# Kernel optimization log

Measured on AMD Instinct MI355X. Metric: run time of the kernel, lower is better.

The kernel has to match this reference:

```python
import jax, jax.numpy as jnp
import numpy as np

RATIOS = [0.9, 0.7, 0.5, 0.3]
EPS = 1e-5


def _layernorm(x, g, b):
    m = jnp.mean(x, axis=-1, keepdims=True)
    v = jnp.mean(jnp.square(x - m), axis=-1, keepdims=True)
    return (x - m) * jax.lax.rsqrt(v + EPS) * g + b


def _stage(x, g, b, W, bias):
    return _layernorm(x, g, b) @ W + bias


def _prune(x, W1, b1, W2, b2, ratio):
    B, N, C = x.shape
    stats = jnp.mean(x, axis=1)                       # (B, C)
    scores = jax.nn.relu(stats @ W1 + b1) @ W2 + b2    # (B, C)
    k = max(1, int(C * ratio))
    _, idx = jax.lax.top_k(jax.lax.stop_gradient(scores), k)  # (B, k)
    hard = jnp.zeros((B, C), scores.dtype).at[jnp.arange(B)[:, None], idx].set(1.0)
    soft = jax.nn.sigmoid(scores)
    # straight-through: forward value == hard, gradient flows through soft
    mask = hard + soft - jax.lax.stop_gradient(soft)
    return x * mask[:, None, :]


def setup_inputs() -> dict:
    key = jax.random.key(0)
    dims = [(96, 96), (96, 192), (192, 384), (384, 768)]
    inp = {}
    ks = jax.random.split(key, 64)
    ki = iter(ks)
    inp["x"] = jax.random.normal(next(ki), (32, 3136, 96), dtype=jnp.float32)
    for i, (din, dout) in enumerate(dims, 1):
        inp[f"s{i}_g"] = jnp.ones((din,), jnp.float32)
        inp[f"s{i}_b"] = jnp.zeros((din,), jnp.float32)
        inp[f"s{i}_W"] = jax.random.normal(next(ki), (din, dout), jnp.float32) * 0.02
        inp[f"s{i}_bias"] = jnp.zeros((dout,), jnp.float32)
        d = dout
        inp[f"p{i}_W1"] = jax.random.normal(next(ki), (d, d // 4), jnp.float32) * 0.02
        inp[f"p{i}_b1"] = jnp.zeros((d // 4,), jnp.float32)
        inp[f"p{i}_W2"] = jax.random.normal(next(ki), (d // 4, d), jnp.float32) * 0.02
        inp[f"p{i}_b2"] = jnp.zeros((d,), jnp.float32)
    inp["H"] = 56
    inp["W"] = 56
    return inp


def reference(x,
              s1_g, s1_b, s1_W, s1_bias, p1_W1, p1_b1, p1_W2, p1_b2,
              s2_g, s2_b, s2_W, s2_bias, p2_W1, p2_b1, p2_W2, p2_b2,
              s3_g, s3_b, s3_W, s3_bias, p3_W1, p3_b1, p3_W2, p3_b2,
              s4_g, s4_b, s4_W, s4_bias, p4_W1, p4_b1, p4_W2, p4_b2,
              H, W):
    x = _stage(x, s1_g, s1_b, s1_W, s1_bias)
    x = _prune(x, p1_W1, p1_b1, p1_W2, p1_b2, RATIOS[0])
    x = _stage(x, s2_g, s2_b, s2_W, s2_bias)
    x = _prune(x, p2_W1, p2_b1, p2_W2, p2_b2, RATIOS[1])
    x = _stage(x, s3_g, s3_b, s3_W, s3_bias)
    x = _prune(x, p3_W1, p3_b1, p3_W2, p3_b2, RATIOS[2])
    x = _stage(x, s4_g, s4_b, s4_W, s4_bias)
    x = _prune(x, p4_W1, p4_b1, p4_W2, p4_b2, RATIOS[3])
    return x
```

## Files before the change

### kernel.cpp

```cpp
#include <hip/hip_runtime.h>
#include <hip/hip_bf16.h>
#include <stdint.h>

#define NTOK 3136
#define MTOT 100352
#define RPW  14
#define WPB  224

typedef __attribute__((ext_vector_type(8))) short bf16x8;
typedef __attribute__((ext_vector_type(4))) float f32x4;
typedef __attribute__((ext_vector_type(2))) float f32x2;

static __device__ __forceinline__ ushort f2bf(float x) {
  union { float f; uint32_t u; } c; c.f = x;
  uint32_t r = (c.u + 0x7FFFu + ((c.u >> 16) & 1u)) >> 16;
  return (ushort)r;
}
static __device__ __forceinline__ float bf2f(ushort h) {
  union { uint32_t u; float f; } c; c.u = ((uint32_t)h) << 16;
  return c.f;
}

template<int DIN, bool WLO>
__global__ __launch_bounds__(256)
void ln_colsum_k(const float* __restrict__ in, const float* __restrict__ gma,
                 const float* __restrict__ bta, ushort* __restrict__ oh,
                 ushort* __restrict__ ol, float* __restrict__ part)
{
  constexpr int P2 = DIN / 2;
  constexpr int T2 = (P2 + 63) / 64;
  const int wid  = (blockIdx.x * 256 + threadIdx.x) >> 6;
  const int lane = threadIdx.x & 63;
  const int b = wid / WPB;
  const int w = wid - b * WPB;

  f32x2 gv[T2], bv[T2], acc[T2];
#pragma unroll
  for (int t = 0; t < T2; ++t) {
    int c2 = lane + 64 * t;
    if (c2 < P2) {
      gv[t] = *(const f32x2*)(gma + 2 * c2);
      bv[t] = *(const f32x2*)(bta + 2 * c2);
    } else { gv[t] = {0.f, 0.f}; bv[t] = {0.f, 0.f}; }
    acc[t] = {0.f, 0.f};
  }

  const size_t rbase = ((size_t)b * NTOK + (size_t)w * RPW) * DIN;
  const float* ip = in + rbase;
  ushort* oph = oh + rbase;
  ushort* opl = ol + rbase;

  for (int j = 0; j < RPW; ++j) {
    f32x2 v[T2];
    float s = 0.f, sq = 0.f;
#pragma unroll
    for (int t = 0; t < T2; ++t) {
      int c2 = lane + 64 * t;
      f32x2 xv = {0.f, 0.f};
      if (c2 < P2) xv = *(const f32x2*)(ip + (size_t)j * DIN + 2 * c2);
      v[t] = xv;
      s  += xv[0] + xv[1];
      sq += xv[0] * xv[0] + xv[1] * xv[1];
    }
#pragma unroll
    for (int off = 1; off < 64; off <<= 1) {
      s  += __shfl_xor(s, off);
      sq += __shfl_xor(sq, off);
    }
    float m   = s / (float)DIN;
    float var = sq / (float)DIN - m * m;
    float r   = 1.f / sqrtf(var + 1e-5f);
#pragma unroll
    for (int t = 0; t < T2; ++t) {
      int c2 = lane + 64 * t;
      if (c2 < P2) {
        float xn0 = (v[t][0] - m) * r * gv[t][0] + bv[t][0];
        float xn1 = (v[t][1] - m) * r * gv[t][1] + bv[t][1];
        ushort h0 = f2bf(xn0), h1 = f2bf(xn1);
        ((uint32_t*)(oph + (size_t)j * DIN))[c2] =
            (uint32_t)h0 | ((uint32_t)h1 << 16);
        if (WLO) {
          ushort l0 = f2bf(xn0 - bf2f(h0)), l1 = f2bf(xn1 - bf2f(h1));
          ((uint32_t*)(opl + (size_t)j * DIN))[c2] =
              (uint32_t)l0 | ((uint32_t)l1 << 16);
        }
        acc[t][0] += xn0;
        acc[t][1] += xn1;
      }
    }
  }
#pragma unroll
  for (int t = 0; t < T2; ++t) {
    int c2 = lane + 64 * t;
    if (c2 < P2) {
      int c = 2 * c2;
      part[((size_t)b * DIN + c) * WPB + w]     = acc[t][0];
      part[((size_t)b * DIN + c + 1) * WPB + w] = acc[t][1];
    }
  }
}

template<int DIN, int DOUT, int SLOTS>
__global__ __launch_bounds__(1024)
void scores_k(const float* __restrict__ part,
              const float* __restrict__ Wt, const float* __restrict__ bias,
              const float* __restrict__ W1, const float* __restrict__ b1,
              const float* __restrict__ W2, const float* __restrict__ b2,
              float* __restrict__ mask, int k)
{
  constexpr int DH  = DOUT / 4;
  constexpr int DH4 = DH / 4;
  constexpr int NSLC = (1024 / DH4 < 64) ? 1024 / DH4 : 64;
  constexpr int RPSC = (DOUT + NSLC - 1) / NSLC;
  constexpr int C4  = DOUT / 4;
  constexpr int NSLD = (1024 / C4 < 64) ? 1024 / C4 : 64;
  constexpr int RPSD = (DH + NSLD - 1) / NSLD;

  __shared__ float xm[DIN];
  __shared__ float st[DOUT];
  __shared__ float h[DH];
  __shared__ float sc[DOUT];
  __shared__ float red[4096];

  const int b = blockIdx.x, tid = threadIdx.x;

  if constexpr (SLOTS == 25) {
    if (tid < DIN) {
      const float* p = part + ((size_t)b * DIN + tid) * 25;
      float s = 0.f;
#pragma unroll
      for (int i = 0; i < 25; ++i) s += p[i];
      xm[tid] = s * (1.f / (float)NTOK);
    }
  } else {
    const int cg = tid >> 2, wq = tid & 3;
    if (cg < DIN) {
      const float* p = part + ((size_t)b * DIN + cg) * WPB + wq * 56;
      f32x4 a = {0.f, 0.f, 0.f, 0.f};
#pragma unroll
      for (int u = 0; u < 14; ++u) {
        f32x4 t0 = *(const f32x4*)(p + u * 4);
        a[0] += t0[0]; a[1] += t0[1]; a[2] += t0[2]; a[3] += t0[3];
      }
      red[wq * DIN + cg] = (a[0] + a[1]) + (a[2] + a[3]);
    }
    __syncthreads();
    if (tid < DIN)
      xm[tid] = ((red[0 * DIN + tid] + red[1 * DIN + tid]) +
                 (red[2 * DIN + tid] + red[3 * DIN + tid])) * (1.f / (float)NTOK);
  }
  __syncthreads();

  {
    constexpr int RPS = DIN / 4;
    const int j4 = tid % C4, sl = tid / C4;
    if (sl < 4) {
      const float* wp = Wt + (size_t)(sl * RPS) * DOUT + j4 * 4;
      f32x4 acc = {0.f, 0.f, 0.f, 0.f};
#pragma unroll
      for (int r = 0; r < RPS; ++r) {
        f32x4 wv = *(const f32x4*)(wp + (size_t)r * DOUT);
        float xv = xm[sl * RPS + r];
        acc[0] = fmaf(xv, wv[0], acc[0]);
        acc[1] = fmaf(xv, wv[1], acc[1]);
        acc[2] = fmaf(xv, wv[2], acc[2]);
        acc[3] = fmaf(xv, wv[3], acc[3]);
      }
      *(f32x4*)&red[sl * DOUT + j4 * 4] = acc;
    }
  }
  __syncthreads();
  if (tid < DOUT)
    st[tid] = ((red[0 * DOUT + tid] + red[1 * DOUT + tid]) +
               (red[2 * DOUT + tid] + red[3 * DOUT + tid])) + bias[tid];
  __syncthreads();

  {
    const int j4 = tid % DH4, sl = tid / DH4;
    if (sl < NSLC) {
      f32x4 acc = {0.f, 0.f, 0.f, 0.f};
#pragma unroll
      for (int rr = 0; rr < RPSC; ++rr) {
        int r = sl * RPSC + rr;
        if (r < DOUT) {
          f32x4 wv = *(const f32x4*)(W1 + (size_t)r * DH + j4 * 4);
          float sv = st[r];
          acc[0] = fmaf(sv, wv[0], acc[0]);
          acc[1] = fmaf(sv, wv[1], acc[1]);
          acc[2] = fmaf(sv, wv[2], acc[2]);
          acc[3] = fmaf(sv, wv[3], acc[3]);
        }
      }
      *(f32x4*)&red[(size_t)sl * DH + j4 * 4] = acc;
    }
  }
  __syncthreads();
  if (tid < DH) {
    float a = 0.f;
#pragma unroll 4
    for (int sl = 0; sl < NSLC; ++sl) a += red[(size_t)sl * DH + tid];
    h[tid] = fmaxf(b1[tid] + a, 0.f);
  }
  __syncthreads();

  {
    const int c4 = tid % C4, sl = tid / C4;
    if (sl < NSLD) {
      f32x4 acc = {0.f, 0.f, 0.f, 0.f};
#pragma unroll
      for (int rr = 0; rr < RPSD; ++rr) {
        int r = sl * RPSD + rr;
        if (r < DH) {
          f32x4 wv = *(const f32x4*)(W2 + (size_t)r * DOUT + c4 * 4);
          float hv = h[r];
          acc[0] = fmaf(hv, wv[0], acc[0]);
          acc[1] = fmaf(hv, wv[1], acc[1]);
          acc[2] = fmaf(hv, wv[2], acc[2]);
          acc[3] = fmaf(hv, wv[3], acc[3]);
        }
      }
      *(f32x4*)&red[(size_t)sl * DOUT + c4 * 4] = acc;
    }
  }
  __syncthreads();
  for (int c = tid; c < DOUT; c += 1024) {
    float a = 0.f;
#pragma unroll 4
    for (int sl = 0; sl < NSLD; ++sl) a += red[(size_t)sl * DOUT + c];
    sc[c] = b2[c] + a;
  }
  __syncthreads();

  for (int c = tid; c < DOUT; c += 1024) {
    float v = sc[c];
    int rank = 0;
#pragma unroll 8
    for (int j = 0; j < DOUT; ++j) {
      float u = sc[j];
      rank += (u > v) || (u == v && j < c);
    }
    mask[(size_t)b * DOUT + c] = (rank < k) ? 1.f : 0.f;
  }
}

__global__ __launch_bounds__(256)
void convW_all_k(const float* __restrict__ W0, const float* __restrict__ W1,
                 const float* __restrict__ W2, const float* __restrict__ W3,
                 ushort* __restrict__ hi, ushort* __restrict__ lo)
{
  const int Kd[4]   = { 96, 96, 192, 384 };
  const int Nd[4]   = { 96, 192, 384, 768 };
  const int off[5]  = { 0, 12288, 36864, 110592, 405504 };
  const float* Wp[4] = { W0, W1, W2, W3 };

  int idx = blockIdx.x * 256 + threadIdx.x;
  if (idx >= 405504) return;
  int s = (idx >= off[1]) + (idx >= off[2]) + (idx >= off[3]);
  int local = idx - off[s];
  int K = Kd[s], N = Nd[s];
  int n = local / K, kk = local - n * K;
  float v = (n < N) ? Wp[s][(size_t)kk * N + n] : 0.f;
  ushort h = f2bf(v);
  hi[idx] = h;
  lo[idx] = f2bf(v - bf2f(h));
}

#define ASYNC16(GP, LP) __builtin_amdgcn_global_load_lds( \
    (const __attribute__((address_space(1))) void*)(GP),  \
    (__attribute__((address_space(3))) void*)(LP), 16, 0, 0)

template<int K, int NSEG, int BNL, int N, int NWN, bool WLO>
__global__ __launch_bounds__(128 * NWN)
void gemm_ln_k(const ushort* __restrict__ a0, const ushort* __restrict__ a1,
               const ushort* __restrict__ a2,
               const ushort* __restrict__ b0, const ushort* __restrict__ b1,
               const ushort* __restrict__ b2,
               const float* __restrict__ bias, const float* __restrict__ msk,
               const float* __restrict__ gnext, const float* __restrict__ bnext,
               ushort* __restrict__ oh, ushort* __restrict__ ol,
               float* __restrict__ part)
{
  constexpr int T   = 128 * NWN;
  constexpr int R   = T / 4;
  constexpr int AI  = 128 / R;
  constexpr int BI  = BNL / R;
  constexpr int IS  = AI + BI;
  constexpr int WN  = N / NWN;
  constexpr int NFR = WN / 16;
  constexpr int KSTEPS = K / 32;
  constexpr int NT  = NSEG * KSTEPS;
  __shared__ __align__(16) ushort ldsA[3][128 * 32];
  __shared__ __align__(16) ushort ldsB[3][BNL * 32];

  const int tid  = threadIdx.x;
  const int lane = tid & 63;
  const int wid  = tid >> 6;
  const int wm = wid & 1, wn = wid >> 1;

  const int q8  = gridDim.x >> 3;
  const int bid = blockIdx.x;
  const int mt  = (bid & 7) * q8 + (bid >> 3);
  const size_t row0 = (size_t)mt * 128;

  const ushort* Aseg[3] = { a0, a1, a2 };
  const ushort* Bseg[3] = { b0, b1, b2 };

  f32x4 acc[4][NFR];
#pragma unroll
  for (int i = 0; i < 4; ++i)
#pragma unroll
    for (int j = 0; j < NFR; ++j) acc[i][j] = { 0.f, 0.f, 0.f, 0.f };

  const int c_row  = tid >> 2;
  const int c_phys = tid & 3;

#define STAGEF(BUF, TT)                                                        \
  {                                                                            \
    const int seg_ = (TT) / KSTEPS;                                            \
    const int k0_  = ((TT) % KSTEPS) * 32;                                     \
    const ushort* ap_ = Aseg[seg_];                                            \
    const ushort* bp_ = Bseg[seg_];                                            \
    _Pragma("unroll")                                                          \
    for (int r_ = 0; r_ < AI; ++r_) {                                          \
      int row_  = c_row + r_ * R;                                              \
      int slot_ = c_phys ^ ((row_ >> 1) & 3);                                  \
      ASYNC16(ap_ + (row0 + row_) * (size_t)K + (k0_ + slot_ * 8),             \
              &ldsA[BUF][(row_ * 4 + c_phys) * 8]);                            \
    }                                                                          \
    _Pragma("unroll")                                                          \
    for (int r_ = 0; r_ < BI; ++r_) {                                          \
      int row_  = c_row + r_ * R;                                              \
      int slot_ = c_phys ^ ((row_ >> 1) & 3);                                  \
      ASYNC16(bp_ + (size_t)row_ * K + (k0_ + slot_ * 8),                      \
              &ldsB[BUF][(row_ * 4 + c_phys) * 8]);                            \
    }                                                                          \
  }

  STAGEF(0, 0);
  STAGEF(1, 1);
#pragma unroll
  for (int t = 0; t < NT; ++t) {
    if (t == NT - 1)            { asm volatile("s_waitcnt vmcnt(0)" ::: "memory"); }
    else if constexpr (IS == 4) { asm volatile("s_waitcnt vmcnt(4)" ::: "memory"); }
    else                        { asm volatile("s_waitcnt vmcnt(5)" ::: "memory"); }
    __builtin_amdgcn_s_barrier();
    if (t + 2 < NT) STAGEF((t + 2) % 3, t + 2);
    const int buf = t % 3;
    const int slot = lane >> 4;
    const int r16  = lane & 15;
    bf16x8 af[4], bfr[NFR];
#pragma unroll
    for (int mi = 0; mi < 4; ++mi) {
      int r = wm * 64 + mi * 16 + r16;
      af[mi] = *(const bf16x8*)&ldsA[buf][(r * 4 + (slot ^ ((r >> 1) & 3))) * 8];
    }
#pragma unroll
    for (int ni = 0; ni < NFR; ++ni) {
      int r = wn * WN + ni * 16 + r16;
      bfr[ni] = *(const bf16x8*)&ldsB[buf][(r * 4 + (slot ^ ((r >> 1) & 3))) * 8];
    }
#pragma unroll
    for (int mi = 0; mi < 4; ++mi)
#pragma unroll
      for (int ni = 0; ni < NFR; ++ni)
        acc[mi][ni] = __builtin_amdgcn_mfma_f32_16x16x32_bf16(af[mi], bfr[ni],
                                                              acc[mi][ni], 0, 0, 0);
  }
#undef STAGEF

  __syncthreads();

  float* rowred = (float*)&ldsA[0][0];
  float* colred = rowred + NWN * 256;
  ushort* xsh = (ushort*)&ldsB[0][0];
  ushort* xsl = xsh + 32 * N;

  const int l15 = lane & 15, l4 = lane >> 4;
  const int b0i = (int)(row0 / NTOK);
  const size_t rowB = (size_t)(b0i + 1) * NTOK;
  const bool strad = rowB < row0 + 128;

  float biasv[NFR], mk0a[NFR], mk1a[NFR], gvn[NFR], bvn[NFR];
#pragma unroll
  for (int ni = 0; ni < NFR; ++ni) {
    int n = wn * WN + ni * 16 + l15;
    biasv[ni] = bias[n];
    mk0a[ni] = msk[(size_t)b0i * N + n];
    mk1a[ni] = strad ? msk[(size_t)(b0i + 1) * N + n] : mk0a[ni];
    gvn[ni] = gnext[n];
    bvn[ni] = bnext[n];
  }

  float rs[16], rq[16];
#pragma unroll
  for (int i = 0; i < 16; ++i) { rs[i] = 0.f; rq[i] = 0.f; }
#pragma unroll
  for (int mi = 0; mi < 4; ++mi)
#pragma unroll
    for (int q = 0; q < 4; ++q) {
      size_t row = row0 + wm * 64 + mi * 16 + l4 * 4 + q;
      bool loB = row < rowB;
#pragma unroll
      for (int ni = 0; ni < NFR; ++ni) {
        float v = (acc[mi][ni][q] + biasv[ni]) * (loB ? mk0a[ni] : mk1a[ni]);
        acc[mi][ni][q] = v;
        rs[mi * 4 + q] += v;
        rq[mi * 4 + q] += v * v;
      }
    }
#pragma unroll
  for (int off = 1; off < 16; off <<= 1)
#pragma unroll
    for (int i = 0; i < 16; ++i) {
      rs[i] += __shfl_xor(rs[i], off);
      rq[i] += __shfl_xor(rq[i], off);
    }
  if (l15 == 0) {
#pragma unroll
    for (int mi = 0; mi < 4; ++mi)
#pragma unroll
      for (int q = 0; q < 4; ++q) {
        int r = wm * 64 + mi * 16 + l4 * 4 + q;
        rowred[(wn * 128 + r) * 2 + 0] = rs[mi * 4 + q];
        rowred[(wn * 128 + r) * 2 + 1] = rq[mi * 4 + q];
      }
  }
  __syncthreads();

  float mean[16], rstd[16];
#pragma unroll
  for (int mi = 0; mi < 4; ++mi)
#pragma unroll
    for (int q = 0; q < 4; ++q) {
      int r = wm * 64 + mi * 16 + l4 * 4 + q;
      float S = 0.f, Q = 0.f;
#pragma unroll
      for (int w = 0; w < NWN; ++w) {
        S += rowred[(w * 128 + r) * 2 + 0];
        Q += rowred[(w * 128 + r) * 2 + 1];
      }
      float mn  = S / (float)N;
      float var = Q / (float)N - mn * mn;
      mean[mi * 4 + q] = mn;
      rstd[mi * 4 + q] = 1.f / sqrtf(var + 1e-5f);
    }

  float cs0[NFR], cs1[NFR];
#pragma unroll
  for (int ni = 0; ni < NFR; ++ni) { cs0[ni] = 0.f; cs1[ni] = 0.f; }
#pragma unroll
  for (int mi = 0; mi < 4; ++mi) {
    __syncthreads();
#pragma unroll
    for (int q = 0; q < 4; ++q) {
      const int rl = l4 * 4 + q;
      const size_t row = row0 + wm * 64 + mi * 16 + rl;
      const bool loB = row < rowB;
      const float mn = mean[mi * 4 + q], rv = rstd[mi * 4 + q];
#pragma unroll
      for (int ni = 0; ni < NFR; ++ni) {
        const int n = wn * WN + ni * 16 + l15;
        float xn = (acc[mi][ni][q] - mn) * rv * gvn[ni] + bvn[ni];
        ushort hh = f2bf(xn);
        xsh[(wm * 16 + rl) * N + n] = hh;
        if constexpr (WLO) xsl[(wm * 16 + rl) * N + n] = f2bf(xn - bf2f(hh));
        if (loB) cs0[ni] += xn; else cs1[ni] += xn;
      }
    }
    __syncthreads();
    constexpr int U4R = N / 8;
    for (int idx = tid; idx < 32 * U4R; idx += T) {
      const int grp = idx / U4R, c = idx - grp * U4R;
      const size_t row = row0 + (grp >> 4) * 64 + mi * 16 + (grp & 15);
      *(uint4*)(oh + row * (size_t)N + c * 8) =
          *(const uint4*)(xsh + grp * N + c * 8);
      if constexpr (WLO)
        *(uint4*)(ol + row * (size_t)N + c * 8) =
            *(const uint4*)(xsl + grp * N + c * 8);
    }
  }

#pragma unroll
  for (int ni = 0; ni < NFR; ++ni) {
    cs0[ni] += __shfl_xor(cs0[ni], 16);
    cs0[ni] += __shfl_xor(cs0[ni], 32);
    cs1[ni] += __shfl_xor(cs1[ni], 16);
    cs1[ni] += __shfl_xor(cs1[ni], 32);
  }
  __syncthreads();
  if (l4 == 0) {
#pragma unroll
    for (int ni = 0; ni < NFR; ++ni) {
      int n = wn * WN + ni * 16 + l15;
      colred[(0 * 2 + wm) * N + n] = cs0[ni];
      colred[(1 * 2 + wm) * N + n] = cs1[ni];
    }
  }
  __syncthreads();
  if (wm == 0 && l4 == 0) {
    const int mt_lo = (b0i * NTOK) >> 7;
    const int slot0 = mt - mt_lo;
#pragma unroll
    for (int ni = 0; ni < NFR; ++ni) {
      int n = wn * WN + ni * 16 + l15;
      float t0 = colred[0 * N + n] + colred[1 * N + n];
      part[((size_t)b0i * N + n) * 25 + slot0] = t0;
      if (strad) {
        float t1 = colred[2 * N + n] + colred[3 * N + n];
        part[((size_t)(b0i + 1) * N + n) * 25 + 0] = t1;
      }
    }
  }
}

template<int K, int NSEG, int BN>
__global__ __launch_bounds__(256)
void gemm_mfma_k(const ushort* __restrict__ a0, const ushort* __restrict__ a1,
                 const ushort* __restrict__ a2,
                 const ushort* __restrict__ b0, const ushort* __restrict__ b1,
                 const ushort* __restrict__ b2,
                 const float* __restrict__ bias, const float* __restrict__ msk,
                 float* __restrict__ C, int N)
{
  constexpr int KSTEPS = K / 32;
  constexpr int NT  = NSEG * KSTEPS;
  constexpr int WN  = BN / 2;
  constexpr int NFR = WN / 16;
  constexpr int BR  = BN / 64;
  __shared__ __align__(16) ushort ldsA[3][128 * 32];
  __shared__ __align__(16) ushort ldsB[3][BN * 32];

  const int tid  = threadIdx.x;
  const int lane = tid & 63;
  const int wid  = tid >> 6;
  const int wm = wid >> 1, wn = wid & 1;

  const int NBN = (N + BN - 1) / BN;
  const int q8  = gridDim.x >> 3;
  const int bid = blockIdx.x;
  const int wg  = (bid & 7) * q8 + (bid >> 3);
  const int mt  = wg / NBN;
  const int nt  = wg - mt * NBN;
  const size_t row0 = (size_t)mt * 128;
  const int n0 = nt * BN;

  const ushort* Aseg[3] = { a0, a1, a2 };
  const ushort* Bseg[3] = { b0, b1, b2 };

  f32x4 acc[4][NFR];
#pragma unroll
  for (int i = 0; i < 4; ++i)
#pragma unroll
    for (int j = 0; j < NFR; ++j) acc[i][j] = { 0.f, 0.f, 0.f, 0.f };

  const int c_row  = tid >> 2;
  const int c_phys = tid & 3;

#define STAGE4(BUF, TT)                                                        \
  {                                                                            \
    const int seg_ = (TT) / KSTEPS;                                            \
    const int k0_  = ((TT) % KSTEPS) * 32;                                     \
    const ushort* ap_ = Aseg[seg_];                                            \
    const ushort* bp_ = Bseg[seg_];                                            \
    _Pragma("unroll")                                                          \
    for (int r_ = 0; r_ < 2; ++r_) {                                           \
      int row_  = c_row + r_ * 64;                                             \
      int slot_ = c_phys ^ ((row_ >> 1) & 3);                                  \
      ASYNC16(ap_ + (row0 + row_) * (size_t)K + (k0_ + slot_ * 8),             \
              &ldsA[BUF][(row_ * 4 + c_phys) * 8]);                            \
    }                                                                          \
    _Pragma("unroll")                                                          \
    for (int r_ = 0; r_ < BR; ++r_) {                                          \
      int row_  = c_row + r_ * 64;                                             \
      int slot_ = c_phys ^ ((row_ >> 1) & 3);                                  \
      ASYNC16(bp_ + (size_t)(n0 + row_) * K + (k0_ + slot_ * 8),               \
              &ldsB[BUF][(row_ * 4 + c_phys) * 8]);                            \
    }                                                                          \
  }

  STAGE4(0, 0);
  STAGE4(1, 1);
#pragma unroll
  for (int t = 0; t < NT; ++t) {
    if (t == NT - 1)              { asm volatile("s_waitcnt vmcnt(0)" ::: "memory"); }
    else if constexpr (BN == 128) { asm volatile("s_waitcnt vmcnt(4)" ::: "memory"); }
    else if constexpr (BN == 192) { asm volatile("s_waitcnt vmcnt(5)" ::: "memory"); }
    else                          { asm volatile("s_waitcnt vmcnt(6)" ::: "memory"); }
    __builtin_amdgcn_s_barrier();
    if (t + 2 < NT) STAGE4((t + 2) % 3, t + 2);
    const int buf = t % 3;
    const int slot = lane >> 4;
    const int r16  = lane & 15;
    bf16x8 af[4], bfr[NFR];
#pragma unroll
    for (int mi = 0; mi < 4; ++mi) {
      int r = wm * 64 + mi * 16 + r16;
      af[mi] = *(const bf16x8*)&ldsA[buf][(r * 4 + (slot ^ ((r >> 1) & 3))) * 8];
    }
#pragma unroll
    for (int ni = 0; ni < NFR; ++ni) {
      int r = wn * WN + ni * 16 + r16;
      bfr[ni] = *(const bf16x8*)&ldsB[buf][(r * 4 + (slot ^ ((r >> 1) & 3))) * 8];
    }
#pragma unroll
    for (int mi = 0; mi < 4; ++mi)
#pragma unroll
      for (int ni = 0; ni < NFR; ++ni)
        acc[mi][ni] = __builtin_amdgcn_mfma_f32_16x16x32_bf16(af[mi], bfr[ni],
                                                              acc[mi][ni], 0, 0, 0);
  }
#undef STAGE4

  float* cst = (float*)&ldsB[0][0];

  const int l15 = lane & 15, l4 = lane >> 4;
  const int b0i = (int)(row0 / NTOK);
  const size_t rowB = (size_t)(b0i + 1) * NTOK;
  const bool straddle = (rowB < row0 + 128) && (b0i + 1 < 32);

  float biasv[NFR], mk0a[NFR], mk1a[NFR];
#pragma unroll
  for (int ni = 0; ni < NFR; ++ni) {
    int n = n0 + wn * WN + ni * 16 + l15;
    biasv[ni] = bias[n];
    mk0a[ni] = msk[(size_t)b0i * N + n];
    mk1a[ni] = straddle ? msk[(size_t)(b0i + 1) * N + n] : mk0a[ni];
  }

#pragma unroll
  for (int mi = 0; mi < 4; ++mi) {
    __syncthreads();
#pragma unroll
    for (int q = 0; q < 4; ++q) {
      const int rl = l4 * 4 + q;
      const size_t m = row0 + wm * 64 + mi * 16 + rl;
      const bool loB = m < rowB;
#pragma unroll
      for (int ni = 0; ni < NFR; ++ni) {
        const int nn = wn * WN + ni * 16 + l15;
        cst[(wm * 16 + rl) * BN + nn] =
            (acc[mi][ni][q] + biasv[ni]) * (loB ? mk0a[ni] : mk1a[ni]);
      }
    }
    __syncthreads();
    constexpr int F4R = BN / 4;
    for (int idx = tid; idx < 32 * F4R; idx += 256) {
      const int grp = idx / F4R, c = idx - grp * F4R;
      const size_t row = row0 + (grp >> 4) * 64 + mi * 16 + (grp & 15);
      *(f32x4*)(C + row * (size_t)N + n0 + c * 4) =
          *(const f32x4*)(cst + grp * BN + c * 4);
    }
  }
}

extern "C" void kernel_launch(void* const* d_in, const int* in_sizes, int n_in,
                              void* d_out, int out_size, void* d_ws, size_t ws_size,
                              hipStream_t stream)
{
  (void)in_sizes; (void)n_in; (void)out_size; (void)ws_size;
  const float* x = (const float*)d_in[0];
  const float *sg[4], *sb[4], *sW[4], *sbias[4], *pW1[4], *pb1[4], *pW2[4], *pb2[4];
  for (int s = 0; s < 4; ++s) {
    int base = 1 + s * 8;
    sg[s]    = (const float*)d_in[base + 0];
    sb[s]    = (const float*)d_in[base + 1];
    sW[s]    = (const float*)d_in[base + 2];
    sbias[s] = (const float*)d_in[base + 3];
    pW1[s]   = (const float*)d_in[base + 4];
    pb1[s]   = (const float*)d_in[base + 5];
    pW2[s]   = (const float*)d_in[base + 6];
    pb2[s]   = (const float*)d_in[base + 7];
  }

  float* out = (float*)d_out;
  ushort* hiA = (ushort*)out;
  ushort* loA = (ushort*)(out + 19267584);
  ushort* loB = (ushort*)(out + 38535168);

  char* ws = (char*)d_ws;
  ushort* hiB  = (ushort*)(ws);
  float*  part = (float*) (ws + 77070336);
  float*  mk   = (float*) (ws + 79822848);
  ushort* w_hi = (ushort*)(ws + 79921152);
  ushort* w_lo = (ushort*)(ws + 80732160);

  const int woff[4] = { 0, 12288, 36864, 110592 };

  convW_all_k<<<(405504 + 255) / 256, 256, 0, stream>>>(
      sW[0], sW[1], sW[2], sW[3], w_hi, w_lo);

  const int LNG = 32 * WPB / 4;

  ln_colsum_k<96, true><<<LNG, 256, 0, stream>>>(x, sg[0], sb[0], hiA, loA, part);
  scores_k<96, 96, 224><<<32, 1024, 0, stream>>>(part, sW[0], sbias[0],
      pW1[0], pb1[0], pW2[0], pb2[0], mk, 86);
  gemm_ln_k<96, 3, 128, 96, 2, true><<<784, 256, 0, stream>>>(
      hiA, hiA, loA, w_hi + woff[0], w_lo + woff[0], w_hi + woff[0],
      sbias[0], mk, sg[1], sb[1], hiB, loB, part);

  scores_k<96, 192, 25><<<32, 1024, 0, stream>>>(part, sW[1], sbias[1],
      pW1[1], pb1[1], pW2[1], pb2[1], mk, 134);
  gemm_ln_k<96, 3, 192, 192, 2, true><<<784, 256, 0, stream>>>(
      hiB, hiB, loB, w_hi + woff[1], w_lo + woff[1], w_hi + woff[1],
      sbias[1], mk, sg[2], sb[2], hiA, loA, part);

  scores_k<192, 384, 25><<<32, 1024, 0, stream>>>(part, sW[2], sbias[2],
      pW1[2], pb1[2], pW2[2], pb2[2], mk, 192);
  gemm_ln_k<192, 3, 384, 384, 4, false><<<784, 512, 0, stream>>>(
      hiA, hiA, loA, w_hi + woff[2], w_lo + woff[2], w_hi + woff[2],
      sbias[2], mk, sg[3], sb[3], hiB, (ushort*)nullptr, part);

  scores_k<384, 768, 25><<<32, 1024, 0, stream>>>(part, sW[3], sbias[3],
      pW1[3], pb1[3], pW2[3], pb2[3], mk, 230);
  gemm_mfma_k<384, 1, 256><<<784 * 3, 256, 0, stream>>>(
      hiB, hiB, hiB, w_hi + woff[3], w_hi + woff[3], w_hi + woff[3],
      sbias[3], mk, out, 768);
}
```

Baseline: 550.7 us.

## Compute only the selected top-k output channels in the final stage GEMM

Result: faster. 490.3 us (-11.0%).

```diff
diff --git a/kernel.cpp b/kernel.cpp
--- a/kernel.cpp
+++ b/kernel.cpp
@@ -100,13 +100,15 @@
   }
 }
 
-template<int DIN, int DOUT, int SLOTS>
+template<int DIN, int DOUT, int SLOTS, bool CMP>
 __global__ __launch_bounds__(1024)
 void scores_k(const float* __restrict__ part,
               const float* __restrict__ Wt, const float* __restrict__ bias,
               const float* __restrict__ W1, const float* __restrict__ b1,
               const float* __restrict__ W2, const float* __restrict__ b2,
-              float* __restrict__ mask, int k)
+              float* __restrict__ mask, int k,
+              const ushort* __restrict__ wsrc, ushort* __restrict__ wc,
+              int* __restrict__ list_g, float* __restrict__ biasc)
 {
   constexpr int DH  = DOUT / 4;
   constexpr int DH4 = DH / 4;
@@ -121,6 +123,7 @@
   __shared__ float h[DH];
   __shared__ float sc[DOUT];
   __shared__ float red[4096];
+  __shared__ int lsh[256];
 
   const int b = blockIdx.x, tid = threadIdx.x;
 
@@ -240,6 +243,24 @@
       rank += (u > v) || (u == v && j < c);
     }
     mask[(size_t)b * DOUT + c] = (rank < k) ? 1.f : 0.f;
+    if (CMP && rank < k) lsh[rank] = c;
+  }
+  if constexpr (CMP) {
+    if (tid >= k && tid < 256) lsh[tid] = -1;
+    __syncthreads();
+    if (tid < 256) {
+      int c = lsh[tid];
+      list_g[b * 256 + tid] = c;
+      biasc[b * 256 + tid] = (c >= 0) ? bias[c] : 0.f;
+    }
+    constexpr int U4 = 384 / 8;
+    for (int idx = tid; idx < 256 * U4; idx += 1024) {
+      int j = idx / U4, u = idx - j * U4;
+      int src = lsh[j];
+      uint4 v = make_uint4(0u, 0u, 0u, 0u);
+      if (src >= 0) v = *(const uint4*)(wsrc + (size_t)src * 384 + u * 8);
+      *(uint4*)(wc + (size_t)b * 98304 + (size_t)j * 384 + u * 8) = v;
+    }
   }
 }
 
@@ -371,9 +392,9 @@
   __syncthreads();
 
   float* rowred = (float*)&ldsA[0][0];
-  float* colred = rowred + NWN * 256;
   ushort* xsh = (ushort*)&ldsB[0][0];
   ushort* xsl = xsh + 32 * N;
+  float* colred = (float*)(xsh + 32 * N * (WLO ? 2 : 1));
 
   const int l15 = lane & 15, l4 = lane >> 4;
   const int b0i = (int)(row0 / NTOK);
@@ -513,142 +534,130 @@
   }
 }
 
-template<int K, int NSEG, int BN>
-__global__ __launch_bounds__(256)
-void gemm_mfma_k(const ushort* __restrict__ a0, const ushort* __restrict__ a1,
-                 const ushort* __restrict__ a2,
-                 const ushort* __restrict__ b0, const ushort* __restrict__ b1,
-                 const ushort* __restrict__ b2,
-                 const float* __restrict__ bias, const float* __restrict__ msk,
-                 float* __restrict__ C, int N)
+template<int K>
+__global__ __launch_bounds__(512)
+void gemm_c4_k(const ushort* __restrict__ A, const ushort* __restrict__ Wc,
+               const int* __restrict__ list, const float* __restrict__ biasc,
+               float* __restrict__ C)
 {
-  constexpr int KSTEPS = K / 32;
-  constexpr int NT  = NSEG * KSTEPS;
-  constexpr int WN  = BN / 2;
-  constexpr int NFR = WN / 16;
-  constexpr int BR  = BN / 64;
+  constexpr int NT = K / 32;
   __shared__ __align__(16) ushort ldsA[3][128 * 32];
-  __shared__ __align__(16) ushort ldsB[3][BN * 32];
+  __shared__ __align__(16) ushort ldsB[3][256 * 32];
 
   const int tid  = threadIdx.x;
   const int lane = tid & 63;
   const int wid  = tid >> 6;
-  const int wm = wid >> 1, wn = wid & 1;
-
-  const int NBN = (N + BN - 1) / BN;
+  const int wm = wid & 1, wn = wid >> 1;
+
   const int q8  = gridDim.x >> 3;
   const int bid = blockIdx.x;
   const int wg  = (bid & 7) * q8 + (bid >> 3);
-  const int mt  = wg / NBN;
-  const int nt  = wg - mt * NBN;
-  const size_t row0 = (size_t)mt * 128;
-  const int n0 = nt * BN;
-
-  const ushort* Aseg[3] = { a0, a1, a2 };
-  const ushort* Bseg[3] = { b0, b1, b2 };
-
-  f32x4 acc[4][NFR];
-#pragma unroll
-  for (int i = 0; i < 4; ++i)
-#pragma unroll
-    for (int j = 0; j < NFR; ++j) acc[i][j] = { 0.f, 0.f, 0.f, 0.f };
+  const int b   = wg / 25;
+  const int mt  = wg - b * 25;
+  const size_t row0 = (size_t)b * NTOK + (size_t)mt * 128;
+  const int rows_valid = (mt == 24) ? 64 : 128;
+
+  const ushort* bp = Wc + (size_t)b * 256 * K;
 
   const int c_row  = tid >> 2;
   const int c_phys = tid & 3;
 
-#define STAGE4(BUF, TT)                                                        \
+  size_t arow = row0 + c_row;
+  const size_t rowEnd = (size_t)(b + 1) * NTOK;
+  if (arow >= rowEnd) arow = rowEnd - 1;
+  const ushort* apr = A + arow * (size_t)K;
+
+  f32x4 acc[4][4];
+#pragma unroll
+  for (int i = 0; i < 4; ++i)
+#pragma unroll
+    for (int j = 0; j < 4; ++j) acc[i][j] = { 0.f, 0.f, 0.f, 0.f };
+
+#define STAGEC(BUF, TT)                                                        \
   {                                                                            \
-    const int seg_ = (TT) / KSTEPS;                                            \
-    const int k0_  = ((TT) % KSTEPS) * 32;                                     \
-    const ushort* ap_ = Aseg[seg_];                                            \
-    const ushort* bp_ = Bseg[seg_];                                            \
+    const int k0_ = (TT) * 32;                                                 \
+    {                                                                          \
+      int slot_ = c_phys ^ ((c_row >> 1) & 3);                                 \
+      ASYNC16(apr + (k0_ + slot_ * 8),                                         \
+              &ldsA[BUF][(c_row * 4 + c_phys) * 8]);                           \
+    }                                                                          \
     _Pragma("unroll")                                                          \
     for (int r_ = 0; r_ < 2; ++r_) {                                           \
-      int row_  = c_row + r_ * 64;                                             \
+      int row_  = c_row + r_ * 128;                                            \
       int slot_ = c_phys ^ ((row_ >> 1) & 3);                                  \
-      ASYNC16(ap_ + (row0 + row_) * (size_t)K + (k0_ + slot_ * 8),             \
-              &ldsA[BUF][(row_ * 4 + c_phys) * 8]);                            \
-    }                                                                          \
-    _Pragma("unroll")                                                          \
-    for (int r_ = 0; r_ < BR; ++r_) {                                          \
-      int row_  = c_row + r_ * 64;                                             \
-      int slot_ = c_phys ^ ((row_ >> 1) & 3);                                  \
-      ASYNC16(bp_ + (size_t)(n0 + row_) * K + (k0_ + slot_ * 8),               \
+      ASYNC16(bp + (size_t)row_ * K + (k0_ + slot_ * 8),                       \
               &ldsB[BUF][(row_ * 4 + c_phys) * 8]);                            \
     }                                                                          \
   }
 
-  STAGE4(0, 0);
-  STAGE4(1, 1);
+  STAGEC(0, 0);
+  STAGEC(1, 1);
 #pragma unroll
   for (int t = 0; t < NT; ++t) {
-    if (t == NT - 1)              { asm volatile("s_waitcnt vmcnt(0)" ::: "memory"); }
-    else if constexpr (BN == 128) { asm volatile("s_waitcnt vmcnt(4)" ::: "memory"); }
-    else if constexpr (BN == 192) { asm volatile("s_waitcnt vmcnt(5)" ::: "memory"); }
-    else                          { asm volatile("s_waitcnt vmcnt(6)" ::: "memory"); }
+    if (t == NT - 1) { asm volatile("s_waitcnt vmcnt(0)" ::: "memory"); }
+    else             { asm volatile("s_waitcnt vmcnt(3)" ::: "memory"); }
     __builtin_amdgcn_s_barrier();
-    if (t + 2 < NT) STAGE4((t + 2) % 3, t + 2);
+    if (t + 2 < NT) STAGEC((t + 2) % 3, t + 2);
     const int buf = t % 3;
     const int slot = lane >> 4;
     const int r16  = lane & 15;
-    bf16x8 af[4], bfr[NFR];
+    bf16x8 af[4], bfr[4];
 #pragma unroll
     for (int mi = 0; mi < 4; ++mi) {
       int r = wm * 64 + mi * 16 + r16;
       af[mi] = *(const bf16x8*)&ldsA[buf][(r * 4 + (slot ^ ((r >> 1) & 3))) * 8];
     }
 #pragma unroll
-    for (int ni = 0; ni < NFR; ++ni) {
-      int r = wn * WN + ni * 16 + r16;
+    for (int ni = 0; ni < 4; ++ni) {
+      int r = wn * 64 + ni * 16 + r16;
       bfr[ni] = *(const bf16x8*)&ldsB[buf][(r * 4 + (slot ^ ((r >> 1) & 3))) * 8];
     }
 #pragma unroll
     for (int mi = 0; mi < 4; ++mi)
 #pragma unroll
-      for (int ni = 0; ni < NFR; ++ni)
+      for (int ni = 0; ni < 4; ++ni)
         acc[mi][ni] = __builtin_amdgcn_mfma_f32_16x16x32_bf16(af[mi], bfr[ni],
                                                               acc[mi][ni], 0, 0, 0);
   }
-#undef STAGE4
+#undef STAGEC
 
   float* cst = (float*)&ldsB[0][0];
 
   const int l15 = lane & 15, l4 = lane >> 4;
-  const int b0i = (int)(row0 / NTOK);
-  const size_t rowB = (size_t)(b0i + 1) * NTOK;
-  const bool straddle = (rowB < row0 + 128) && (b0i + 1 < 32);
-
-  float biasv[NFR], mk0a[NFR], mk1a[NFR];
-#pragma unroll
-  for (int ni = 0; ni < NFR; ++ni) {
-    int n = n0 + wn * WN + ni * 16 + l15;
-    biasv[ni] = bias[n];
-    mk0a[ni] = msk[(size_t)b0i * N + n];
-    mk1a[ni] = straddle ? msk[(size_t)(b0i + 1) * N + n] : mk0a[ni];
-  }
-
-#pragma unroll
-  for (int mi = 0; mi < 4; ++mi) {
+  int   nj[4];
+  float biasv[4];
+#pragma unroll
+  for (int ni = 0; ni < 4; ++ni) {
+    int j = wn * 64 + ni * 16 + l15;
+    nj[ni]    = list[b * 256 + j];
+    biasv[ni] = biasc[b * 256 + j];
+  }
+
+#pragma unroll
+  for (int hh = 0; hh < 8; ++hh) {
+    const int hrows = rows_valid - hh * 16;
+    if (hrows <= 0) break;
     __syncthreads();
-#pragma unroll
-    for (int q = 0; q < 4; ++q) {
-      const int rl = l4 * 4 + q;
-      const size_t m = row0 + wm * 64 + mi * 16 + rl;
-      const bool loB = m < rowB;
-#pragma unroll
-      for (int ni = 0; ni < NFR; ++ni) {
-        const int nn = wn * WN + ni * 16 + l15;
-        cst[(wm * 16 + rl) * BN + nn] =
-            (acc[mi][ni][q] + biasv[ni]) * (loB ? mk0a[ni] : mk1a[ni]);
-      }
-    }
+    for (int idx = tid; idx < 16 * 192; idx += 512)
+      ((f32x4*)cst)[idx] = f32x4{0.f, 0.f, 0.f, 0.f};
     __syncthreads();
-    constexpr int F4R = BN / 4;
-    for (int idx = tid; idx < 32 * F4R; idx += 256) {
-      const int grp = idx / F4R, c = idx - grp * F4R;
-      const size_t row = row0 + (grp >> 4) * 64 + mi * 16 + (grp & 15);
-      *(f32x4*)(C + row * (size_t)N + n0 + c * 4) =
-          *(const f32x4*)(cst + grp * BN + c * 4);
+    if ((hh >> 2) == wm) {
+      const int mi = hh & 3;
+#pragma unroll
+      for (int q = 0; q < 4; ++q) {
+        const int rl = l4 * 4 + q;
+#pragma unroll
+        for (int ni = 0; ni < 4; ++ni)
+          if (nj[ni] >= 0)
+            cst[rl * 768 + nj[ni]] = acc[mi][ni][q] + biasv[ni];
+      }
+    }
+    __syncthreads();
+    const int nst = (hrows >= 16 ? 16 : hrows) * 192;
+    for (int idx = tid; idx < nst; idx += 512) {
+      const int grp = idx / 192, c = idx - grp * 192;
+      const size_t row = row0 + hh * 16 + grp;
+      *(f32x4*)(C + row * 768 + c * 4) = ((const f32x4*)cst)[grp * 192 + c];
     }
   }
 }
@@ -683,6 +692,9 @@
   float*  mk   = (float*) (ws + 79822848);
   ushort* w_hi = (ushort*)(ws + 79921152);
   ushort* w_lo = (ushort*)(ws + 80732160);
+  ushort* wc   = (ushort*)(ws + 81543168);
+  int*    lst  = (int*)   (ws + 87834624);
+  float*  bsc  = (float*) (ws + 87867392);
 
   const int woff[4] = { 0, 12288, 36864, 110592 };
 
@@ -692,27 +704,25 @@
   const int LNG = 32 * WPB / 4;
 
   ln_colsum_k<96, true><<<LNG, 256, 0, stream>>>(x, sg[0], sb[0], hiA, loA, part);
-  scores_k<96, 96, 224><<<32, 1024, 0, stream>>>(part, sW[0], sbias[0],
-      pW1[0], pb1[0], pW2[0], pb2[0], mk, 86);
+  scores_k<96, 96, 224, false><<<32, 1024, 0, stream>>>(part, sW[0], sbias[0],
+      pW1[0], pb1[0], pW2[0], pb2[0], mk, 86, nullptr, nullptr, nullptr, nullptr);
   gemm_ln_k<96, 3, 128, 96, 2, true><<<784, 256, 0, stream>>>(
       hiA, hiA, loA, w_hi + woff[0], w_lo + woff[0], w_hi + woff[0],
       sbias[0], mk, sg[1], sb[1], hiB, loB, part);
 
-  scores_k<96, 192, 25><<<32, 1024, 0, stream>>>(part, sW[1], sbias[1],
-      pW1[1], pb1[1], pW2[1], pb2[1], mk, 134);
+  scores_k<96, 192, 25, false><<<32, 1024, 0, stream>>>(part, sW[1], sbias[1],
+      pW1[1], pb1[1], pW2[1], pb2[1], mk, 134, nullptr, nullptr, nullptr, nullptr);
   gemm_ln_k<96, 3, 192, 192, 2, true><<<784, 256, 0, stream>>>(
       hiB, hiB, loB, w_hi + woff[1], w_lo + woff[1], w_hi + woff[1],
       sbias[1], mk, sg[2], sb[2], hiA, loA, part);
 
-  scores_k<192, 384, 25><<<32, 1024, 0, stream>>>(part, sW[2], sbias[2],
-      pW1[2], pb1[2], pW2[2], pb2[2], mk, 192);
+  scores_k<192, 384, 25, false><<<32, 1024, 0, stream>>>(part, sW[2], sbias[2],
+      pW1[2], pb1[2], pW2[2], pb2[2], mk, 192, nullptr, nullptr, nullptr, nullptr);
   gemm_ln_k<192, 3, 384, 384, 4, false><<<784, 512, 0, stream>>>(
       hiA, hiA, loA, w_hi + woff[2], w_lo + woff[2], w_hi + woff[2],
       sbias[2], mk, sg[3], sb[3], hiB, (ushort*)nullptr, part);
 
-  scores_k<384, 768, 25><<<32, 1024, 0, stream>>>(part, sW[3], sbias[3],
-      pW1[3], pb1[3], pW2[3], pb2[3], mk, 230);
-  gemm_mfma_k<384, 1, 256><<<784 * 3, 256, 0, stream>>>(
-      hiB, hiB, hiB, w_hi + woff[3], w_hi + woff[3], w_hi + woff[3],
-      sbias[3], mk, out, 768);
+  scores_k<384, 768, 25, true><<<32, 1024, 0, stream>>>(part, sW[3], sbias[3],
+      pW1[3], pb1[3], pW2[3], pb2[3], mk, 230, w_hi + woff[3], wc, lst, bsc);
+  gemm_c4_k<384><<<800, 512, 0, stream>>>(hiB, wc, lst, bsc, out);
 }
```
